# Kernel tuning notes

Measured on AMD Instinct MI355X. Metric: run time of the kernel, lower is better.

## Reference

```python
import jax, jax.numpy as jnp
import numpy as np

N_NODES = 50000
N_EDGES = 600000
C_IN = 128
C_OUT = 128
LN_EPS = 1e-5


def _multi_aggr(x, edge_index, num_nodes):
    """4-way scatter aggregate: returns [N, 4*C] = concat(mean, max, min, sum).
    Matches PyG semantics: empty segments produce 0 for all reducers."""
    src, dst = edge_index[0], edge_index[1]
    msgs = x[src]                                              # [E, C]
    s = jax.ops.segment_sum(msgs, dst, num_segments=num_nodes)  # [N, C]
    cnt = jax.ops.segment_sum(jnp.ones((msgs.shape[0],), x.dtype), dst,
                              num_segments=num_nodes)           # [N]
    has = (cnt > 0)[:, None]
    mean = s / jnp.maximum(cnt, 1.0)[:, None]
    mx = jax.ops.segment_max(msgs, dst, num_segments=num_nodes)
    mn = jax.ops.segment_min(msgs, dst, num_segments=num_nodes)
    mx = jnp.where(has, mx, 0.0)
    mn = jnp.where(has, mn, 0.0)
    return jnp.concatenate([mean, mx, mn, s], axis=-1)         # [N, 4C]


def setup_inputs() -> dict:
    key = jax.random.key(0)
    ks = jax.random.split(key, 8)
    x = jax.random.normal(ks[0], (N_NODES, C_IN), dtype=jnp.float32)
    ei1 = jax.random.randint(ks[1], (2, N_EDGES), 0, N_NODES, dtype=jnp.int32)
    ei2 = jax.random.randint(ks[2], (2, N_EDGES), 0, N_NODES, dtype=jnp.int32)
    # Xavier-ish scaled weights (torch Linear stores [out, in])
    W1_r1 = jax.random.normal(ks[3], (C_OUT, C_IN), dtype=jnp.float32) * (1.0 / np.sqrt(C_IN))
    W2_r1 = jax.random.normal(ks[4], (C_OUT, 4 * C_IN), dtype=jnp.float32) * (1.0 / np.sqrt(4 * C_IN))
    W1_r2 = jax.random.normal(ks[5], (C_OUT, C_IN), dtype=jnp.float32) * (1.0 / np.sqrt(C_IN))
    W2_r2 = jax.random.normal(ks[6], (C_OUT, 4 * C_IN), dtype=jnp.float32) * (1.0 / np.sqrt(4 * C_IN))
    gamma = jnp.ones((C_OUT,), dtype=jnp.float32)
    beta = jnp.zeros((C_OUT,), dtype=jnp.float32)
    return {"x": x, "edge_index_r1": ei1, "edge_index_r2": ei2,
            "W1_r1": W1_r1, "W2_r1": W2_r1, "W1_r2": W1_r2, "W2_r2": W2_r2,
            "gamma": gamma, "beta": beta}


def reference(x, edge_index_r1, edge_index_r2, W1_r1, W2_r1, W1_r2, W2_r2, gamma, beta):
    n = x.shape[0]
    s1 = _multi_aggr(x, edge_index_r1, n)                      # [N, 4C]
    s2 = _multi_aggr(x, edge_index_r2, n)                      # [N, 4C]
    h_r1 = x @ W1_r1.T + s1 @ W2_r1.T                          # [N, C_OUT]
    h_r2 = x @ W1_r2.T + s2 @ W2_r2.T                          # [N, C_OUT]
    h = jax.nn.relu(0.5 * (h_r1 + h_r2))                       # mean over 2 relations + relu
    mu = jnp.mean(h, axis=-1, keepdims=True)
    var = jnp.mean((h - mu) ** 2, axis=-1, keepdims=True)
    return (h - mu) * jax.lax.rsqrt(var + LN_EPS) * gamma + beta
```

## Files before the change

kernel.cpp:

```cpp
#include <hip/hip_runtime.h>
#include <stdint.h>

#define N_NODES 50000
#define N_EDGES 600000
#define M_PAD   50048
#define NXCD    8
#define REG_SZ  6250
#define CAP     48
#define ESLICE  2048
#define NSLICE  293
#define FILL_BLKS (NSLICE * NXCD * 2)

typedef __bf16 bf16x8 __attribute__((ext_vector_type(8)));
typedef float  f32x4  __attribute__((ext_vector_type(4)));

__device__ __forceinline__ unsigned short f2bf(float f) {
  union { float f; unsigned u; } v; v.f = f;
  unsigned r = v.u + 0x7FFF + ((v.u >> 16) & 1);
  return (unsigned short)(r >> 16);
}

__device__ __forceinline__ unsigned cvt_pk_bf16(float lo, float hi) {
  unsigned r;
  asm("v_cvt_pk_bf16_f32 %0, %1, %2" : "=v"(r) : "v"(lo), "v"(hi));
  return r;
}

__global__ void phase1_kernel(const int* __restrict__ ei1, const int* __restrict__ ei2,
                              int* __restrict__ cnt1, int* __restrict__ cnt2,
                              unsigned short* __restrict__ csr1, unsigned short* __restrict__ csr2,
                              const float* __restrict__ x, unsigned short* __restrict__ xb,
                              const float* __restrict__ W1a, const float* __restrict__ W2a,
                              const float* __restrict__ W1b, const float* __restrict__ W2b,
                              unsigned short* __restrict__ Bm) {
  int b = blockIdx.x;
  if (b < FILL_BLKS) {
    int region = b & (NXCD - 1);
    int sid = b >> 3;
    int rel = (sid >= NSLICE);
    int slice = rel ? sid - NSLICE : sid;
    const int* ei = rel ? ei2 : ei1;
    int* cnt = rel ? cnt2 : cnt1;
    unsigned short* csr = rel ? csr2 : csr1;
    int lo = region * REG_SZ;
    int base = slice * ESLICE + threadIdx.x;
    #pragma unroll
    for (int k = 0; k < ESLICE / 256; ++k) {
      int i = base + k * 256;
      if (i < N_EDGES) {
        int d = ei[N_EDGES + i];
        if ((unsigned)(d - lo) < (unsigned)REG_SZ) {
          int r = atomicAdd(&cnt[d], 1);
          if (r < CAP) csr[d * CAP + r] = (unsigned short)ei[i];
        }
      }
    }
  } else if (b < 4688 + 6250) {
    int i = (b - 4688) * 256 + threadIdx.x;
    if (i < N_NODES * 32) {
      float4 v = ((const float4*)x)[i];
      unsigned lo = cvt_pk_bf16(v.x, v.y);
      unsigned hi = cvt_pk_bf16(v.z, v.w);
      ((uint2*)xb)[i] = make_uint2(lo, hi);
    }
  } else {
    int i = (b - 10938) * 256 + threadIdx.x;
    if (i < 128 * 1152) {
      int n = i / 1152, k = i % 1152;
      float v;
      if (k < 128)      v = W1a[n * 128 + k] + W1b[n * 128 + k];
      else if (k < 640) v = W2a[n * 512 + (k - 128)];
      else              v = W2b[n * 512 + (k - 640)];
      Bm[i] = f2bf(v);
    }
  }
}

__global__ void aggregate_kernel(const unsigned short* __restrict__ xb,
                                 const unsigned short* __restrict__ csr,
                                 const int* __restrict__ cnt,
                                 unsigned short* __restrict__ s) {
  int wid = blockIdx.x * 4 + (threadIdx.x >> 6);
  int lane = threadIdx.x & 63;
  if (wid >= N_NODES) return;
  int deg = cnt[wid];
  if (deg > CAP) deg = CAP;
  unsigned* row = (unsigned*)(s + (size_t)wid * 512) + lane;
  if (deg == 0) {
    row[0] = 0u; row[64] = 0u; row[128] = 0u; row[192] = 0u;
    return;
  }
  int beg = wid * CAP, end = beg + deg;

  const unsigned* xl = (const unsigned*)xb + lane;

  float s0 = 0.f, s1v = 0.f;
  float mx0 = -3.0e38f, mx1 = -3.0e38f;
  float mn0 = 3.0e38f, mn1 = 3.0e38f;

  int e = beg;
  int i0 = csr[e];
  int i1 = (e + 1 < end) ? csr[e + 1] : i0;
  int i2 = (e + 2 < end) ? csr[e + 2] : i0;
  int i3 = (e + 3 < end) ? csr[e + 3] : i0;
  int i4 = (e + 4 < end) ? csr[e + 4] : i0;
  int i5 = (e + 5 < end) ? csr[e + 5] : i0;
  int i6 = (e + 6 < end) ? csr[e + 6] : i0;
  int i7 = (e + 7 < end) ? csr[e + 7] : i0;

  while (e + 7 < end) {
    unsigned u0 = xl[(unsigned)i0 << 6];
    unsigned u1 = xl[(unsigned)i1 << 6];
    unsigned u2 = xl[(unsigned)i2 << 6];
    unsigned u3 = xl[(unsigned)i3 << 6];
    unsigned u4 = xl[(unsigned)i4 << 6];
    unsigned u5 = xl[(unsigned)i5 << 6];
    unsigned u6 = xl[(unsigned)i6 << 6];
    unsigned u7 = xl[(unsigned)i7 << 6];
    int en = e + 8;
    i0 = csr[(en     < end) ? en     : beg];
    i1 = csr[(en + 1 < end) ? en + 1 : beg];
    i2 = csr[(en + 2 < end) ? en + 2 : beg];
    i3 = csr[(en + 3 < end) ? en + 3 : beg];
    i4 = csr[(en + 4 < end) ? en + 4 : beg];
    i5 = csr[(en + 5 < end) ? en + 5 : beg];
    i6 = csr[(en + 6 < end) ? en + 6 : beg];
    i7 = csr[(en + 7 < end) ? en + 7 : beg];
    float a0 = __uint_as_float(u0 << 16), a1 = __uint_as_float(u0 & 0xFFFF0000u);
    float b0 = __uint_as_float(u1 << 16), b1 = __uint_as_float(u1 & 0xFFFF0000u);
    float c0 = __uint_as_float(u2 << 16), c1 = __uint_as_float(u2 & 0xFFFF0000u);
    float d0 = __uint_as_float(u3 << 16), d1 = __uint_as_float(u3 & 0xFFFF0000u);
    float e0 = __uint_as_float(u4 << 16), e1 = __uint_as_float(u4 & 0xFFFF0000u);
    float f0 = __uint_as_float(u5 << 16), f1 = __uint_as_float(u5 & 0xFFFF0000u);
    float g0 = __uint_as_float(u6 << 16), g1 = __uint_as_float(u6 & 0xFFFF0000u);
    float h0 = __uint_as_float(u7 << 16), h1 = __uint_as_float(u7 & 0xFFFF0000u);
    s0  += ((a0 + b0) + (c0 + d0)) + ((e0 + f0) + (g0 + h0));
    s1v += ((a1 + b1) + (c1 + d1)) + ((e1 + f1) + (g1 + h1));
    mx0 = fmaxf(fmaxf(fmaxf(a0, b0), c0), fmaxf(fmaxf(fmaxf(d0, e0), f0), fmaxf(fmaxf(g0, h0), mx0)));
    mx1 = fmaxf(fmaxf(fmaxf(a1, b1), c1), fmaxf(fmaxf(fmaxf(d1, e1), f1), fmaxf(fmaxf(g1, h1), mx1)));
    mn0 = fminf(fminf(fminf(a0, b0), c0), fminf(fminf(fminf(d0, e0), f0), fminf(fminf(g0, h0), mn0)));
    mn1 = fminf(fminf(fminf(a1, b1), c1), fminf(fminf(fminf(d1, e1), f1), fminf(fminf(g1, h1), mn1)));
    e = en;
  }
  int rem = end - e;
  if (rem >= 4) {
    unsigned u0 = xl[(unsigned)i0 << 6];
    unsigned u1 = xl[(unsigned)i1 << 6];
    unsigned u2 = xl[(unsigned)i2 << 6];
    unsigned u3 = xl[(unsigned)i3 << 6];
    float a0 = __uint_as_float(u0 << 16), a1 = __uint_as_float(u0 & 0xFFFF0000u);
    float b0 = __uint_as_float(u1 << 16), b1 = __uint_as_float(u1 & 0xFFFF0000u);
    float c0 = __uint_as_float(u2 << 16), c1 = __uint_as_float(u2 & 0xFFFF0000u);
    float d0 = __uint_as_float(u3 << 16), d1 = __uint_as_float(u3 & 0xFFFF0000u);
    s0  += (a0 + b0) + (c0 + d0);
    s1v += (a1 + b1) + (c1 + d1);
    mx0 = fmaxf(fmaxf(a0, b0), fmaxf(fmaxf(c0, d0), mx0));
    mx1 = fmaxf(fmaxf(a1, b1), fmaxf(fmaxf(c1, d1), mx1));
    mn0 = fminf(fminf(a0, b0), fminf(fminf(c0, d0), mn0));
    mn1 = fminf(fminf(a1, b1), fminf(fminf(c1, d1), mn1));
    i0 = i4; i1 = i5; i2 = i6;
    rem -= 4;
  }
  if (rem >= 2) {
    unsigned u0 = xl[(unsigned)i0 << 6];
    unsigned u1 = xl[(unsigned)i1 << 6];
    float a0 = __uint_as_float(u0 << 16), a1 = __uint_as_float(u0 & 0xFFFF0000u);
    float b0 = __uint_as_float(u1 << 16), b1 = __uint_as_float(u1 & 0xFFFF0000u);
    s0 += a0 + b0;  s1v += a1 + b1;
    mx0 = fmaxf(fmaxf(a0, b0), mx0);  mx1 = fmaxf(fmaxf(a1, b1), mx1);
    mn0 = fminf(fminf(a0, b0), mn0);  mn1 = fminf(fminf(a1, b1), mn1);
    i0 = i2;
    rem -= 2;
  }
  if (rem >= 1) {
    unsigned u0 = xl[(unsigned)i0 << 6];
    float a0 = __uint_as_float(u0 << 16), a1 = __uint_as_float(u0 & 0xFFFF0000u);
    s0 += a0;  s1v += a1;
    mx0 = fmaxf(mx0, a0);  mx1 = fmaxf(mx1, a1);
    mn0 = fminf(mn0, a0);  mn1 = fminf(mn1, a1);
  }

  float inv = 1.0f / (float)deg;
  row[0]   = cvt_pk_bf16(s0 * inv, s1v * inv);
  row[64]  = cvt_pk_bf16(mx0, mx1);
  row[128] = cvt_pk_bf16(mn0, mn1);
  row[192] = cvt_pk_bf16(s0, s1v);
}

__device__ __forceinline__ void gload16(void* lds, const void* g) {
  __builtin_amdgcn_global_load_lds(
      (const __attribute__((address_space(1))) char*)g,
      (__attribute__((address_space(3))) char*)lds, 16, 0, 0);
}

__global__ __launch_bounds__(256) void gemm_ln_kernel(
    const unsigned short* __restrict__ xb, const unsigned short* __restrict__ s1,
    const unsigned short* __restrict__ s2, const unsigned short* __restrict__ Bm,
    const float* __restrict__ gamma, const float* __restrict__ beta,
    float* __restrict__ out) {
  __shared__ __align__(16) unsigned short As[64 * 64];
  __shared__ __align__(16) unsigned short Bs[128 * 64];
  __shared__ float rsum[64][2];
  __shared__ float rsq[64][2];

  const int t = threadIdx.x;
  const int lane = t & 63;
  const int wid = t >> 6;
  const int wr = wid >> 1, wc = wid & 1;
  const int m0 = blockIdx.x * 64;

  f32x4 acc[2][4];
  #pragma unroll
  for (int i = 0; i < 2; ++i)
    #pragma unroll
    for (int j = 0; j < 4; ++j) acc[i][j] = {0.f, 0.f, 0.f, 0.f};

  for (int kt = 0; kt < 18; ++kt) {
    const unsigned short* aptr; int astride, kloc;
    if (kt < 2)       { aptr = xb; astride = 128; kloc = kt * 64; }
    else if (kt < 10) { aptr = s1; astride = 512; kloc = (kt - 2) * 64; }
    else              { aptr = s2; astride = 512; kloc = (kt - 10) * 64; }

    #pragma unroll
    for (int i = 0; i < 2; ++i) {
      int chunk = i * 256 + t;
      int r = chunk >> 3, c8 = chunk & 7;
      int c8s = c8 ^ (r & 7);
      gload16(As + chunk * 8, aptr + (size_t)(m0 + r) * astride + kloc + c8s * 8);
    }
    #pragma unroll
    for (int i = 0; i < 4; ++i) {
      int chunk = i * 256 + t;
      int r = chunk >> 3, c8 = chunk & 7;
      int c8s = c8 ^ (r & 7);
      gload16(Bs + chunk * 8, Bm + (size_t)r * 1152 + kt * 64 + c8s * 8);
    }
    __syncthreads();

    #pragma unroll
    for (int kk = 0; kk < 2; ++kk) {
      bf16x8 a[2], b[4];
      int ccb = kk * 4 + (lane >> 4);
      #pragma unroll
      for (int mf = 0; mf < 2; ++mf) {
        int row = wr * 32 + mf * 16 + (lane & 15);
        int swz = ccb ^ (row & 7);
        a[mf] = *(const bf16x8*)(As + row * 64 + swz * 8);
      }
      #pragma unroll
      for (int nf = 0; nf < 4; ++nf) {
        int n = wc * 64 + nf * 16 + (lane & 15);
        int swz = ccb ^ (n & 7);
        b[nf] = *(const bf16x8*)(Bs + n * 64 + swz * 8);
      }
      #pragma unroll
      for (int mf = 0; mf < 2; ++mf)
        #pragma unroll
        for (int nf = 0; nf < 4; ++nf)
          acc[mf][nf] = __builtin_amdgcn_mfma_f32_16x16x32_bf16(a[mf], b[nf], acc[mf][nf], 0, 0, 0);
    }
    __syncthreads();
  }

  float g[4], bta[4];
  #pragma unroll
  for (int nf = 0; nf < 4; ++nf) {
    int n = wc * 64 + nf * 16 + (lane & 15);
    g[nf] = gamma[n]; bta[nf] = beta[n];
  }

  #pragma unroll
  for (int mf = 0; mf < 2; ++mf) {
    #pragma unroll
    for (int r = 0; r < 4; ++r) {
      float ps = 0.f, pq = 0.f;
      #pragma unroll
      for (int nf = 0; nf < 4; ++nf) {
        float v = fmaxf(0.5f * acc[mf][nf][r], 0.0f);
        acc[mf][nf][r] = v;
        ps += v; pq += v * v;
      }
      #pragma unroll
      for (int d = 1; d < 16; d <<= 1) {
        ps += __shfl_xor(ps, d);
        pq += __shfl_xor(pq, d);
      }
      if ((lane & 15) == 0) {
        int m = wr * 32 + mf * 16 + ((lane >> 4) << 2) + r;
        rsum[m][wc] = ps;
        rsq[m][wc] = pq;
      }
    }
  }
  __syncthreads();

  #pragma unroll
  for (int mf = 0; mf < 2; ++mf) {
    #pragma unroll
    for (int r = 0; r < 4; ++r) {
      int m = wr * 32 + mf * 16 + ((lane >> 4) << 2) + r;
      float sum = rsum[m][0] + rsum[m][1];
      float sq  = rsq[m][0] + rsq[m][1];
      float mu = sum * (1.0f / 128.0f);
      float var = fmaxf(sq * (1.0f / 128.0f) - mu * mu, 0.0f);
      float rstd = rsqrtf(var + 1e-5f);
      int mg = m0 + m;
      if (mg < N_NODES) {
        #pragma unroll
        for (int nf = 0; nf < 4; ++nf) {
          int n = wc * 64 + nf * 16 + (lane & 15);
          out[(size_t)mg * 128 + n] = (acc[mf][nf][r] - mu) * rstd * g[nf] + bta[nf];
        }
      }
    }
  }
}

extern "C" void kernel_launch(void* const* d_in, const int* in_sizes, int n_in,
                              void* d_out, int out_size, void* d_ws, size_t ws_size,
                              hipStream_t stream) {
  const float* x    = (const float*)d_in[0];
  const int*   ei1  = (const int*)d_in[1];
  const int*   ei2  = (const int*)d_in[2];
  const float* W1a  = (const float*)d_in[3];
  const float* W2a  = (const float*)d_in[4];
  const float* W1b  = (const float*)d_in[5];
  const float* W2b  = (const float*)d_in[6];
  const float* gamma = (const float*)d_in[7];
  const float* beta  = (const float*)d_in[8];
  float* out = (float*)d_out;

  char* w = (char*)d_ws;
  auto alloc = [&](size_t b) { char* p = w; w += (b + 255) & ~(size_t)255; return p; };
  int* cnt1 = (int*)alloc((size_t)N_NODES * 4);
  int* cnt2 = (int*)alloc((size_t)N_NODES * 4);
  unsigned short* xb = (unsigned short*)alloc((size_t)M_PAD * 128 * 2);
  unsigned short* s1 = (unsigned short*)alloc((size_t)M_PAD * 512 * 2);
  unsigned short* s2 = (unsigned short*)alloc((size_t)M_PAD * 512 * 2);
  unsigned short* Bm = (unsigned short*)alloc((size_t)128 * 1152 * 2);

  unsigned short* csr1 = (unsigned short*)d_out;
  unsigned short* csr2 = csr1 + (size_t)N_NODES * CAP;

  hipMemsetAsync(cnt1, 0, (size_t)2 * N_NODES * 4 + 256, stream);
  phase1_kernel<<<11514, 256, 0, stream>>>(ei1, ei2, cnt1, cnt2, csr1, csr2,
                                           x, xb, W1a, W2a, W1b, W2b, Bm);
  aggregate_kernel<<<12500, 256, 0, stream>>>(xb, csr1, cnt1, s1);
  aggregate_kernel<<<12500, 256, 0, stream>>>(xb, csr2, cnt2, s2);
  gemm_ln_kernel<<<782, 256, 0, stream>>>(xb, s1, s2, Bm, gamma, beta, out);
}
```

Measured before the change: 157.5 us.

## Drop the stored sum aggregate, rebuild it as degree-scaled mean inside the GEMM

The aggregate kernel no longer writes the sum block, so each relation's buffer shrinks from 512 to 384 columns. The GEMM rebuilds the sum term by scaling the mean A-fragment by the node degree and running extra MFMAs against reordered weight columns. It also merges the two aggregate launches into one 2-D grid. This cuts HBM write and read traffic on the intermediates at the cost of extra LDS loads, conversions, MFMA work on four k-tiles, and some added bf16 rounding error.

```diff
diff --git a/kernel.cpp b/kernel.cpp
--- a/kernel.cpp
+++ b/kernel.cpp
@@ -68,26 +68,34 @@
     if (i < 128 * 1152) {
       int n = i / 1152, k = i % 1152;
       float v;
-      if (k < 128)      v = W1a[n * 128 + k] + W1b[n * 128 + k];
-      else if (k < 640) v = W2a[n * 512 + (k - 128)];
-      else              v = W2b[n * 512 + (k - 640)];
+      if (k < 128)       v = W1a[n * 128 + k] + W1b[n * 128 + k];
+      else if (k < 512)  v = W2a[n * 512 + (k - 128)];
+      else if (k < 896)  v = W2b[n * 512 + (k - 512)];
+      else if (k < 1024) v = W2a[n * 512 + 384 + (k - 896)];
+      else               v = W2b[n * 512 + 384 + (k - 1024)];
       Bm[i] = f2bf(v);
     }
   }
 }
 
 __global__ void aggregate_kernel(const unsigned short* __restrict__ xb,
-                                 const unsigned short* __restrict__ csr,
-                                 const int* __restrict__ cnt,
-                                 unsigned short* __restrict__ s) {
+                                 const unsigned short* __restrict__ csr1,
+                                 const int* __restrict__ cnt1,
+                                 unsigned short* __restrict__ sa,
+                                 const unsigned short* __restrict__ csr2,
+                                 const int* __restrict__ cnt2,
+                                 unsigned short* __restrict__ sb) {
+  const unsigned short* csr = blockIdx.y ? csr2 : csr1;
+  const int* cnt = blockIdx.y ? cnt2 : cnt1;
+  unsigned short* s = blockIdx.y ? sb : sa;
   int wid = blockIdx.x * 4 + (threadIdx.x >> 6);
   int lane = threadIdx.x & 63;
   if (wid >= N_NODES) return;
   int deg = cnt[wid];
   if (deg > CAP) deg = CAP;
-  unsigned* row = (unsigned*)(s + (size_t)wid * 512) + lane;
+  unsigned* row = (unsigned*)(s + (size_t)wid * 384) + lane;
   if (deg == 0) {
-    row[0] = 0u; row[64] = 0u; row[128] = 0u; row[192] = 0u;
+    row[0] = 0u; row[64] = 0u; row[128] = 0u;
     return;
   }
   int beg = wid * CAP, end = beg + deg;
@@ -184,7 +192,6 @@
   row[0]   = cvt_pk_bf16(s0 * inv, s1v * inv);
   row[64]  = cvt_pk_bf16(mx0, mx1);
   row[128] = cvt_pk_bf16(mn0, mn1);
-  row[192] = cvt_pk_bf16(s0, s1v);
 }
 
 __device__ __forceinline__ void gload16(void* lds, const void* g) {
@@ -196,10 +203,12 @@
 __global__ __launch_bounds__(256) void gemm_ln_kernel(
     const unsigned short* __restrict__ xb, const unsigned short* __restrict__ s1,
     const unsigned short* __restrict__ s2, const unsigned short* __restrict__ Bm,
+    const int* __restrict__ cnt1, const int* __restrict__ cnt2,
     const float* __restrict__ gamma, const float* __restrict__ beta,
     float* __restrict__ out) {
   __shared__ __align__(16) unsigned short As[64 * 64];
   __shared__ __align__(16) unsigned short Bs[128 * 64];
+  __shared__ __align__(16) unsigned short Bs2[128 * 64];
   __shared__ float rsum[64][2];
   __shared__ float rsq[64][2];
 
@@ -209,17 +218,29 @@
   const int wr = wid >> 1, wc = wid & 1;
   const int m0 = blockIdx.x * 64;
 
+  float dga[2], dgb[2];
+  #pragma unroll
+  for (int mf = 0; mf < 2; ++mf) {
+    int row = m0 + wr * 32 + mf * 16 + (lane & 15);
+    int d1 = cnt1[row]; d1 = (d1 > CAP) ? CAP : d1;
+    int d2 = cnt2[row]; d2 = (d2 > CAP) ? CAP : d2;
+    dga[mf] = (float)d1;
+    dgb[mf] = (float)d2;
+  }
+
   f32x4 acc[2][4];
   #pragma unroll
   for (int i = 0; i < 2; ++i)
     #pragma unroll
     for (int j = 0; j < 4; ++j) acc[i][j] = {0.f, 0.f, 0.f, 0.f};
 
-  for (int kt = 0; kt < 18; ++kt) {
+  for (int kt = 0; kt < 14; ++kt) {
     const unsigned short* aptr; int astride, kloc;
-    if (kt < 2)       { aptr = xb; astride = 128; kloc = kt * 64; }
-    else if (kt < 10) { aptr = s1; astride = 512; kloc = (kt - 2) * 64; }
-    else              { aptr = s2; astride = 512; kloc = (kt - 10) * 64; }
+    if (kt < 2)      { aptr = xb; astride = 128; kloc = kt * 64; }
+    else if (kt < 8) { aptr = s1; astride = 384; kloc = (kt - 2) * 64; }
+    else             { aptr = s2; astride = 384; kloc = (kt - 8) * 64; }
+    bool extra = (kt == 2) | (kt == 3) | (kt == 8) | (kt == 9);
+    int base2 = (kt == 2) ? 896 : (kt == 3) ? 960 : (kt == 8) ? 1024 : 1088;
 
     #pragma unroll
     for (int i = 0; i < 2; ++i) {
@@ -234,6 +255,8 @@
       int r = chunk >> 3, c8 = chunk & 7;
       int c8s = c8 ^ (r & 7);
       gload16(Bs + chunk * 8, Bm + (size_t)r * 1152 + kt * 64 + c8s * 8);
+      if (extra)
+        gload16(Bs2 + chunk * 8, Bm + (size_t)r * 1152 + base2 + c8s * 8);
     }
     __syncthreads();
 
@@ -258,6 +281,26 @@
         #pragma unroll
         for (int nf = 0; nf < 4; ++nf)
           acc[mf][nf] = __builtin_amdgcn_mfma_f32_16x16x32_bf16(a[mf], b[nf], acc[mf][nf], 0, 0, 0);
+
+      if (extra) {
+        bf16x8 b2[4];
+        #pragma unroll
+        for (int nf = 0; nf < 4; ++nf) {
+          int n = wc * 64 + nf * 16 + (lane & 15);
+          int swz = ccb ^ (n & 7);
+          b2[nf] = *(const bf16x8*)(Bs2 + n * 64 + swz * 8);
+        }
+        #pragma unroll
+        for (int mf = 0; mf < 2; ++mf) {
+          float dg = (kt < 8) ? dga[mf] : dgb[mf];
+          bf16x8 as_;
+          #pragma unroll
+          for (int j = 0; j < 8; ++j) as_[j] = (__bf16)((float)a[mf][j] * dg);
+          #pragma unroll
+          for (int nf = 0; nf < 4; ++nf)
+            acc[mf][nf] = __builtin_amdgcn_mfma_f32_16x16x32_bf16(as_, b2[nf], acc[mf][nf], 0, 0, 0);
+        }
+      }
     }
     __syncthreads();
   }
@@ -335,8 +378,8 @@
   int* cnt1 = (int*)alloc((size_t)N_NODES * 4);
   int* cnt2 = (int*)alloc((size_t)N_NODES * 4);
   unsigned short* xb = (unsigned short*)alloc((size_t)M_PAD * 128 * 2);
-  unsigned short* s1 = (unsigned short*)alloc((size_t)M_PAD * 512 * 2);
-  unsigned short* s2 = (unsigned short*)alloc((size_t)M_PAD * 512 * 2);
+  unsigned short* s1 = (unsigned short*)alloc((size_t)M_PAD * 384 * 2);
+  unsigned short* s2 = (unsigned short*)alloc((size_t)M_PAD * 384 * 2);
   unsigned short* Bm = (unsigned short*)alloc((size_t)128 * 1152 * 2);
 
   unsigned short* csr1 = (unsigned short*)d_out;
@@ -345,7 +388,6 @@
   hipMemsetAsync(cnt1, 0, (size_t)2 * N_NODES * 4 + 256, stream);
   phase1_kernel<<<11514, 256, 0, stream>>>(ei1, ei2, cnt1, cnt2, csr1, csr2,
                                            x, xb, W1a, W2a, W1b, W2b, Bm);
-  aggregate_kernel<<<12500, 256, 0, stream>>>(xb, csr1, cnt1, s1);
-  aggregate_kernel<<<12500, 256, 0, stream>>>(xb, csr2, cnt2, s2);
-  gemm_ln_kernel<<<782, 256, 0, stream>>>(xb, s1, s2, Bm, gamma, beta, out);
-}
+  aggregate_kernel<<<dim3(12500, 2), 256, 0, stream>>>(xb, csr1, cnt1, s1, csr2, cnt2, s2);
+  gemm_ln_kernel<<<782, 256, 0, stream>>>(xb, s1, s2, Bm, cnt1, cnt2, gamma, beta, out);
+}
```

Result: no change. 155.8 us, median of 2 (-1.0%).
